# Performance work log

Hardware: AMD Instinct MI355X
Metric: run time of the kernel (lower is better)

## Reference

```python
import jax, jax.numpy as jnp
import numpy as np

B, N, NUM_GT = 8, 512, 64
C, FH, FW = 16, 16, 16
ROI_ZOOM_W, ROI_ZOOM_H = 1.1, 1.1
CLS_ON_HARD = False
ALLOW_LOW_QUALITY = True


def _make_boxes(key, b, n, img=800.0):
    k1, k2, k3, k4 = jax.random.split(key, 4)
    x1 = jax.random.uniform(k1, (b, n)) * img
    y1 = jax.random.uniform(k2, (b, n)) * img
    w = 32.0 + jax.random.uniform(k3, (b, n)) * 224.0
    h = 32.0 + jax.random.uniform(k4, (b, n)) * 224.0
    return jnp.stack([x1, y1, x1 + w, y1 + h], axis=-1)


def setup_inputs() -> dict:
    key = jax.random.key(0)
    kb, kg, kc, kf, ki = jax.random.split(key, 5)
    boxes = _make_boxes(kb, B, N)
    gt_xyxy = _make_boxes(kg, B, NUM_GT)
    gt_cls = jax.random.randint(kc, (B, NUM_GT, 1), 1, C + 1).astype(jnp.float32)
    gt_boxes = jnp.concatenate([gt_xyxy, gt_cls], axis=-1)
    match_pos_flag = jax.random.randint(kf, (B, N), -1, 2).astype(jnp.int32)
    match_gt_id = jax.random.randint(ki, (B, N), 0, NUM_GT)
    match_gt_id = jnp.where(match_pos_flag > 0, match_gt_id, -1)
    return {"boxes": boxes, "gt_boxes": gt_boxes,
            "match_pos_flag": match_pos_flag, "match_gt_id": match_gt_id}


def _take_row(gt_boxes, idx):
    # gather per-batch rows; -1 (unavailable) clamped to 0, masked later by flags
    idx_c = jnp.clip(idx, 0, gt_boxes.shape[1] - 1)
    return jnp.take_along_axis(gt_boxes, idx_c[..., None], axis=1)


def _zoom_boxes(b, sw, sh):
    cx = (b[..., 0] + b[..., 2]) * 0.5
    cy = (b[..., 1] + b[..., 3]) * 0.5
    w = (b[..., 2] - b[..., 0]) * sw
    h = (b[..., 3] - b[..., 1]) * sh
    return jnp.stack([cx - w / 2, cy - h / 2, cx + w / 2, cy + h / 2], axis=-1)


def _encode(boxes, gt_boxes, match_pos_flag, match_gt_id):
    gt_anchor = _take_row(gt_boxes, match_gt_id)          # (B,N,5)
    box_label = gt_anchor[..., 4]                         # (B,N)
    anchors = _zoom_boxes(boxes, ROI_ZOOM_W, ROI_ZOOM_H)
    ax1, ay1, ax2, ay2 = (anchors[..., i] for i in range(4))
    # gt box relative to anchor top-left
    rx1 = gt_anchor[..., 0] - ax1
    ry1 = gt_anchor[..., 1] - ay1
    rx2 = gt_anchor[..., 2] - ax1
    ry2 = gt_anchor[..., 3] - ay1
    rw, rh = rx2 - rx1, ry2 - ry1
    cx, cy = (rx1 + rx2) * 0.5, (ry1 + ry2) * 0.5
    sw = (ax2 - ax1) / FW                                 # (B,N)
    sh = (ay2 - ay1) / FH
    # grids: ind_w varies along last axis, ind_h along second-to-last (square map)
    ind_w = jnp.arange(FW, dtype=jnp.float32)[None, None, None, :]
    ind_h = jnp.arange(FH, dtype=jnp.float32)[None, None, :, None]

    def e(x):  # (B,N) -> (B,N,1,1)
        return x[..., None, None]

    w_sigma = e(rw / 2 / sw)
    h_sigma = e(rh / 2 / sh)
    if ALLOW_LOW_QUALITY:
        w_sig_s, h_sig_s = jnp.maximum(w_sigma, 1.5), jnp.maximum(h_sigma, 1.5)
        w_sig_c, h_sig_c = jnp.maximum(w_sigma, 0.5), jnp.maximum(h_sigma, 0.5)
    else:
        w_sig_s, h_sig_s, w_sig_c, h_sig_c = w_sigma, h_sigma, w_sigma, h_sigma
    pos_w, pos_h = e(cx / sw), e(cy / sh)
    w_term = jnp.square((pos_w - ind_w - 0.5) / w_sig_s)
    h_term = jnp.square((pos_h - ind_h - 0.5) / h_sig_s)
    heat = jnp.exp(-(w_term + h_term))                    # (B,N,FH,FW)
    cond = (jnp.abs(ind_w + 0.5 - pos_w) < w_sig_c) & (jnp.abs(ind_h + 0.5 - pos_h) < h_sig_c)
    heat = jnp.where(cond, heat, 0.0)

    zero = jnp.zeros((B, N, FH, FW), dtype=heat.dtype)
    ox1 = e(rx1 / sw) - (ind_w + 0.5) + zero
    oy1 = e(ry1 / sh) - (ind_h + 0.5) + zero
    ox2 = e(rx2 / sw) - (ind_w + 0.5) + zero
    oy2 = e(ry2 / sh) - (ind_h + 0.5) + zero
    offset = jnp.stack([ox1, oy1, ox2, oy2], axis=2)      # (B,N,4,FH,FW)

    cls_ids = jnp.arange(C, dtype=jnp.float32)[None, None, :, None, None]
    cls_cond = cls_ids == (jnp.abs(box_label)[:, :, None, None, None] - 1.0)
    label_map = jnp.where(cls_cond, heat[:, :, None, :, :], 0.0)  # (B,N,C,FH,FW)

    small = ((sw < 0.01) | (sh < 0.01))[:, :, None, None, None]
    label_map = jnp.where(small, 0.0, label_map)
    offset = jnp.where(small, 0.0, offset)

    non_neg_label = jnp.where(match_pos_flag != 0, box_label, 0.0)
    pos_match = match_pos_flag > 0
    mask_one = pos_match if CLS_ON_HARD else pos_match & (non_neg_label > 0)
    mask = cls_cond[:, :, :, 0, 0] & mask_one[:, :, None]  # (B,N,C)

    label_map = label_map.reshape(-1, C, FW, FH)
    offset = offset.reshape(-1, 4, FW, FH)
    mask = mask.reshape(-1, C)
    return label_map, offset, mask


def reference(boxes, gt_boxes, match_pos_flag, match_gt_id):
    return _encode(boxes, gt_boxes, match_pos_flag, match_gt_id)
```

## Files before the change

### kernel.cpp

```cpp
#include <hip/hip_runtime.h>

#define BB 8
#define NN 512
#define NUM_GT 64
#define CC 16
#define FH 16
#define FW 16

#define LM_FLOATS (BB*NN*CC*FH*FW)
#define OFF_FLOATS (BB*NN*4*FH*FW)

__global__ __launch_bounds__(256) void rcnn_encode_kernel(
    const float* __restrict__ boxes,
    const float* __restrict__ gt_boxes,
    const int*   __restrict__ match_pos_flag,
    const int*   __restrict__ match_gt_id,
    float* __restrict__ out)
{
    const int bn  = blockIdx.x;
    const int b   = bn >> 9;
    const int tid = threadIdx.x;

    __shared__ __align__(16) float heat_lds[FH*FW];

    const float bx1 = boxes[bn*4+0];
    const float by1 = boxes[bn*4+1];
    const float bx2 = boxes[bn*4+2];
    const float by2 = boxes[bn*4+3];

    const int gid  = match_gt_id[bn];
    const int gidc = min(max(gid, 0), NUM_GT-1);
    const float* g = gt_boxes + (size_t)(b*NUM_GT + gidc)*5;
    const float gx1 = g[0], gy1 = g[1], gx2 = g[2], gy2 = g[3], label = g[4];
    const int flag = match_pos_flag[bn];

    const float cx = (bx1 + bx2) * 0.5f;
    const float cy = (by1 + by2) * 0.5f;
    const float zw = (bx2 - bx1) * 1.1f;
    const float zh = (by2 - by1) * 1.1f;
    const float ax1 = cx - zw * 0.5f;
    const float ay1 = cy - zh * 0.5f;
    const float ax2 = cx + zw * 0.5f;
    const float ay2 = cy + zh * 0.5f;

    const float rx1 = gx1 - ax1;
    const float ry1 = gy1 - ay1;
    const float rx2 = gx2 - ax1;
    const float ry2 = gy2 - ay1;
    const float rw  = rx2 - rx1;
    const float rh  = ry2 - ry1;
    const float rcx = (rx1 + rx2) * 0.5f;
    const float rcy = (ry1 + ry2) * 0.5f;
    const float sw  = (ax2 - ax1) / 16.0f;
    const float sh  = (ay2 - ay1) / 16.0f;

    const float w_sigma = (rw * 0.5f) / sw;
    const float h_sigma = (rh * 0.5f) / sh;
    const float w_sig_s = fmaxf(w_sigma, 1.5f);
    const float h_sig_s = fmaxf(h_sigma, 1.5f);
    const float w_sig_c = fmaxf(w_sigma, 0.5f);
    const float h_sig_c = fmaxf(h_sigma, 0.5f);
    const float pos_w = rcx / sw;
    const float pos_h = rcy / sh;
    const bool  small = (sw < 0.01f) || (sh < 0.01f);

    const float ox1v = rx1 / sw;
    const float oy1v = ry1 / sh;
    const float ox2v = rx2 / sw;
    const float oy2v = ry2 / sh;

    {
        const float fw_ = (float)(tid & 15);
        const float fh_ = (float)(tid >> 4);
        const float wt = ((pos_w - fw_) - 0.5f) / w_sig_s;
        const float ht = ((pos_h - fh_) - 0.5f) / h_sig_s;
        const float heat = expf(-(wt*wt + ht*ht));
        const bool cond = (fabsf((fw_ + 0.5f) - pos_w) < w_sig_c) &&
                          (fabsf((fh_ + 0.5f) - pos_h) < h_sig_c);
        heat_lds[tid] = (cond && !small) ? heat : 0.0f;
    }
    __syncthreads();

    const float c_match = fabsf(label) - 1.0f;

    {
        float4* lm = (float4*)out + (size_t)bn * 1024;
        const float4* heat4 = (const float4*)heat_lds;
        #pragma unroll
        for (int k = 0; k < 4; ++k) {
            const int f = k*256 + tid;
            const int c = f >> 6;
            float4 v = make_float4(0.f, 0.f, 0.f, 0.f);
            if ((float)c == c_match) {
                v = heat4[f & 63];
            }
            lm[f] = v;
        }
    }

    {
        float4* of = (float4*)(out + (size_t)LM_FLOATS) + (size_t)bn * 256;
        const int comp  = tid >> 6;
        const int pbase = (tid & 63) << 2;
        float4 v;
        #pragma unroll
        for (int j = 0; j < 4; ++j) {
            const int p = pbase + j;
            const float fw_ = (float)(p & 15);
            const float fh_ = (float)(p >> 4);
            float val;
            if      (comp == 0) val = ox1v - (fw_ + 0.5f);
            else if (comp == 1) val = oy1v - (fh_ + 0.5f);
            else if (comp == 2) val = ox2v - (fw_ + 0.5f);
            else                val = oy2v - (fh_ + 0.5f);
            ((float*)&v)[j] = small ? 0.0f : val;
        }
        of[tid] = v;
    }

    if (tid < CC) {
        const bool pos_match = flag > 0;
        const float nnl = (flag != 0) ? label : 0.0f;
        const bool mask_one = pos_match && (nnl > 0.0f);
        const bool m = ((float)tid == c_match) && mask_one;
        out[(size_t)LM_FLOATS + (size_t)OFF_FLOATS + (size_t)bn*CC + tid] = m ? 1.0f : 0.0f;
    }
}

extern "C" void kernel_launch(void* const* d_in, const int* in_sizes, int n_in,
                              void* d_out, int out_size, void* d_ws, size_t ws_size,
                              hipStream_t stream) {
    const float* boxes          = (const float*)d_in[0];
    const float* gt_boxes       = (const float*)d_in[1];
    const int*   match_pos_flag = (const int*)d_in[2];
    const int*   match_gt_id    = (const int*)d_in[3];
    float* out = (float*)d_out;

    rcnn_encode_kernel<<<BB*NN, 256, 0, stream>>>(
        boxes, gt_boxes, match_pos_flag, match_gt_id, out);
}
```

Baseline: 98.05 us.

## Compute heat in registers per float4 and use nontemporal stores

```diff
diff --git a/kernel.cpp b/kernel.cpp
--- a/kernel.cpp
+++ b/kernel.cpp
@@ -4,11 +4,13 @@
 #define NN 512
 #define NUM_GT 64
 #define CC 16
-#define FH 16
-#define FW 16
+#define FHH 16
+#define FWW 16
 
-#define LM_FLOATS (BB*NN*CC*FH*FW)
-#define OFF_FLOATS (BB*NN*4*FH*FW)
+#define LM_FLOATS (BB*NN*CC*FHH*FWW)
+#define OFF_FLOATS (BB*NN*4*FHH*FWW)
+
+typedef float fx4 __attribute__((ext_vector_type(4)));
 
 __global__ __launch_bounds__(256) void rcnn_encode_kernel(
     const float* __restrict__ boxes,
@@ -20,8 +22,6 @@
     const int bn  = blockIdx.x;
     const int b   = bn >> 9;
     const int tid = threadIdx.x;
-
-    __shared__ __align__(16) float heat_lds[FH*FW];
 
     const float bx1 = boxes[bn*4+0];
     const float by1 = boxes[bn*4+1];
@@ -69,53 +69,55 @@
     const float ox2v = rx2 / sw;
     const float oy2v = ry2 / sh;
 
-    {
-        const float fw_ = (float)(tid & 15);
-        const float fh_ = (float)(tid >> 4);
-        const float wt = ((pos_w - fw_) - 0.5f) / w_sig_s;
-        const float ht = ((pos_h - fh_) - 0.5f) / h_sig_s;
-        const float heat = expf(-(wt*wt + ht*ht));
-        const bool cond = (fabsf((fw_ + 0.5f) - pos_w) < w_sig_c) &&
-                          (fabsf((fh_ + 0.5f) - pos_h) < h_sig_c);
-        heat_lds[tid] = (cond && !small) ? heat : 0.0f;
-    }
-    __syncthreads();
-
     const float c_match = fabsf(label) - 1.0f;
 
+    const float fh_f = (float)((tid & 63) >> 2);
+    const float fw0  = (float)((tid & 3) << 2);
+
     {
-        float4* lm = (float4*)out + (size_t)bn * 1024;
-        const float4* heat4 = (const float4*)heat_lds;
+        fx4* lm = (fx4*)out + (size_t)bn * 1024;
+        const float ht   = ((pos_h - fh_f) - 0.5f) / h_sig_s;
+        const float ht2  = ht * ht;
+        const bool cond_h = fabsf((fh_f + 0.5f) - pos_h) < h_sig_c;
         #pragma unroll
         for (int k = 0; k < 4; ++k) {
             const int f = k*256 + tid;
             const int c = f >> 6;
-            float4 v = make_float4(0.f, 0.f, 0.f, 0.f);
-            if ((float)c == c_match) {
-                v = heat4[f & 63];
+            fx4 v = (fx4)(0.0f);
+            if (((float)c == c_match) && !small) {
+                #pragma unroll
+                for (int j = 0; j < 4; ++j) {
+                    const float fw_ = fw0 + (float)j;
+                    const float wt  = ((pos_w - fw_) - 0.5f) / w_sig_s;
+                    const bool cond = cond_h &&
+                                      (fabsf((fw_ + 0.5f) - pos_w) < w_sig_c);
+                    v[j] = cond ? expf(-(wt*wt + ht2)) : 0.0f;
+                }
             }
-            lm[f] = v;
+            __builtin_nontemporal_store(v, lm + f);
         }
     }
 
     {
-        float4* of = (float4*)(out + (size_t)LM_FLOATS) + (size_t)bn * 256;
-        const int comp  = tid >> 6;
-        const int pbase = (tid & 63) << 2;
-        float4 v;
-        #pragma unroll
-        for (int j = 0; j < 4; ++j) {
-            const int p = pbase + j;
-            const float fw_ = (float)(p & 15);
-            const float fh_ = (float)(p >> 4);
-            float val;
-            if      (comp == 0) val = ox1v - (fw_ + 0.5f);
-            else if (comp == 1) val = oy1v - (fh_ + 0.5f);
-            else if (comp == 2) val = ox2v - (fw_ + 0.5f);
-            else                val = oy2v - (fh_ + 0.5f);
-            ((float*)&v)[j] = small ? 0.0f : val;
+        fx4* of = (fx4*)(out + (size_t)LM_FLOATS) + (size_t)bn * 256;
+        const int comp = tid >> 6;
+        fx4 v;
+        if (small) {
+            v = (fx4)(0.0f);
+        } else if (comp == 0) {
+            #pragma unroll
+            for (int j = 0; j < 4; ++j)
+                v[j] = ox1v - ((fw0 + (float)j) + 0.5f);
+        } else if (comp == 1) {
+            v = (fx4)(oy1v - (fh_f + 0.5f));
+        } else if (comp == 2) {
+            #pragma unroll
+            for (int j = 0; j < 4; ++j)
+                v[j] = ox2v - ((fw0 + (float)j) + 0.5f);
+        } else {
+            v = (fx4)(oy2v - (fh_f + 0.5f));
         }
-        of[tid] = v;
+        __builtin_nontemporal_store(v, of + tid);
     }
 
     if (tid < CC) {
@@ -123,7 +125,8 @@
         const float nnl = (flag != 0) ? label : 0.0f;
         const bool mask_one = pos_match && (nnl > 0.0f);
         const bool m = ((float)tid == c_match) && mask_one;
-        out[(size_t)LM_FLOATS + (size_t)OFF_FLOATS + (size_t)bn*CC + tid] = m ? 1.0f : 0.0f;
+        __builtin_nontemporal_store(m ? 1.0f : 0.0f,
+            out + (size_t)LM_FLOATS + (size_t)OFF_FLOATS + (size_t)bn*CC + tid);
     }
 }
 
```

New measurement: 99.43 us, median of 2. No clear change (+1.4%).
